# Kernel tuning notes

Measured on AMD Instinct MI355X. Metric: run time of the kernel, lower is better.

The kernel has to match this reference:

```python
import jax, jax.numpy as jnp
import numpy as np

N = 100000
E = 1600000
D_IN = 128
D_HID = 128
D_OUT = 128


def _glorot(key, shape):
    fan_in, fan_out = shape[1], shape[0]
    lim = np.sqrt(6.0 / (fan_in + fan_out)).astype(np.float32)
    return jax.random.uniform(key, shape, jnp.float32, -lim, lim)


def setup_inputs() -> dict:
    key = jax.random.key(0)
    ks = jax.random.split(key, 8)
    x = jax.random.normal(ks[0], (N, D_IN), jnp.float32)
    edge_index = jax.random.randint(ks[1], (2, E), 0, N, jnp.int64)
    # SAGEConv params: lin_l acts on aggregated neighbors (has bias), lin_r on root.
    W1l = _glorot(ks[2], (D_HID, D_IN))
    W1r = _glorot(ks[3], (D_HID, D_IN))
    b1 = jnp.zeros((D_HID,), jnp.float32)
    W2l = _glorot(ks[4], (D_OUT, D_HID))
    W2r = _glorot(ks[5], (D_OUT, D_HID))
    b2 = jnp.zeros((D_OUT,), jnp.float32)
    return {"x": x, "edge_index": edge_index,
            "W1l": W1l, "W1r": W1r, "b1": b1,
            "W2l": W2l, "W2r": W2r, "b2": b2}


def _sage_conv(x, src, dst, Wl, Wr, b):
    # mean-aggregate neighbor features j->i, then lin_l(mean) + lin_r(x) + b
    msgs = x[src]                                             # [E, d]
    summed = jax.ops.segment_sum(msgs, dst, num_segments=N)   # [N, d]
    deg = jax.ops.segment_sum(jnp.ones((src.shape[0],), x.dtype), dst,
                              num_segments=N)                 # [N]
    mean = summed / jnp.maximum(deg, 1.0)[:, None]
    return mean @ Wl.T + x @ Wr.T + b


def reference(x, edge_index, W1l, W1r, b1, W2l, W2r, b2):
    src, dst = edge_index[0], edge_index[1]
    h = jax.nn.relu(_sage_conv(x, src, dst, W1l, W1r, b1))
    # dropout p=0.2 is identity in eval mode
    out = _sage_conv(h, src, dst, W2l, W2r, b2)
    return out
```

## Files before the change

### kernel.cpp

```cpp
#include <hip/hip_runtime.h>
#include <hip/hip_bf16.h>

#define N_NODES 100000
#define N_EDGES 1600000
#define D 128
#define NBUCK 782
#define BSTRIDE 2560
#define EPB 4096

typedef __attribute__((ext_vector_type(8))) short short8v;
typedef __attribute__((ext_vector_type(4))) float f32x4;

__device__ __forceinline__ unsigned short f2bf(float f) {
    unsigned int u = __float_as_uint(f);
    unsigned int r = (u + 0x7fffu + ((u >> 16) & 1u)) >> 16;
    return (unsigned short)r;
}
__device__ __forceinline__ float bf2f(unsigned int lo16) {
    return __uint_as_float(lo16 << 16);
}
__device__ __forceinline__ short8v zero8() {
    short8v z = {0, 0, 0, 0, 0, 0, 0, 0};
    return z;
}
__device__ __forceinline__ short8v cvt8(const float4 p0, const float4 p1) {
    union { __hip_bfloat162 h[4]; short8v s; } u;
    u.h[0] = __float22bfloat162_rn(make_float2(p0.x, p0.y));
    u.h[1] = __float22bfloat162_rn(make_float2(p0.z, p0.w));
    u.h[2] = __float22bfloat162_rn(make_float2(p1.x, p1.y));
    u.h[3] = __float22bfloat162_rn(make_float2(p1.z, p1.w));
    return u.s;
}

__global__ __launch_bounds__(256) void k_bscatter(const int* __restrict__ src,
                                                  const int* __restrict__ dst,
                                                  int* __restrict__ gcnt,
                                                  unsigned int* __restrict__ ebuf) {
    __shared__ int cnt[NBUCK];
    __shared__ int base[NBUCK];
    const int t = threadIdx.x;
    const int e0 = blockIdx.x * EPB;
    for (int i = t; i < NBUCK; i += 256) cnt[i] = 0;
    __syncthreads();
    unsigned int pay[16];
    int meta[16];
#pragma unroll
    for (int u = 0; u < 16; ++u) {
        int e = e0 + u * 256 + t;
        if (e < N_EDGES) {
            int d = dst[e];
            int b = d >> 7;
            int r = atomicAdd(&cnt[b], 1);
            meta[u] = (b << 16) | r;
            pay[u] = ((unsigned int)(d & 127) << 17) | (unsigned int)src[e];
        } else meta[u] = -1;
    }
    __syncthreads();
    for (int i = t; i < NBUCK; i += 256) {
        int c = cnt[i];
        base[i] = c ? atomicAdd(&gcnt[i], c) : 0;
    }
    __syncthreads();
#pragma unroll
    for (int u = 0; u < 16; ++u) {
        if (meta[u] >= 0) {
            int b = meta[u] >> 16;
            int r = meta[u] & 0xffff;
            ebuf[b * BSTRIDE + base[b] + r] = pay[u];
        }
    }
}

__global__ __launch_bounds__(256) void k_bsort(const unsigned int* __restrict__ ebuf,
                                               const int* __restrict__ gcnt,
                                               int* __restrict__ row_start,
                                               int* __restrict__ ssrc) {
    __shared__ int h[128];
    __shared__ int sc[128];
    const int b = blockIdx.x;
    const int t = threadIdx.x;
    const int eb = b * BSTRIDE;
    const int n = gcnt[b];
    if (t < 128) h[t] = 0;
    __syncthreads();
    unsigned int pay[BSTRIDE / 256];
    int meta[BSTRIDE / 256];
#pragma unroll
    for (int u = 0; u < BSTRIDE / 256; ++u) {
        int e = t + u * 256;
        if (e < n) {
            unsigned int pk = ebuf[eb + e];
            int dl = pk >> 17;
            int r = atomicAdd(&h[dl], 1);
            meta[u] = (dl << 16) | r;
            pay[u] = pk;
        } else meta[u] = -1;
    }
    __syncthreads();
    if (t < 128) sc[t] = h[t];
    __syncthreads();
    for (int o = 1; o < 128; o <<= 1) {
        int add = 0;
        if (t < 128 && t >= o) add = sc[t - o];
        __syncthreads();
        if (t < 128) sc[t] += add;
        __syncthreads();
    }
    if (t < 128) {
        int excl = sc[t] - h[t];
        row_start[b * 129 + t] = eb + excl;
        sc[t] = excl;
    }
    if (t == 0) row_start[b * 129 + 128] = eb + n;
    __syncthreads();
#pragma unroll
    for (int u = 0; u < BSTRIDE / 256; ++u) {
        if (meta[u] >= 0) {
            int dl = meta[u] >> 16;
            int r = meta[u] & 0xffff;
            ssrc[eb + sc[dl] + r] = (int)(pay[u] & 0x1ffffu);
        }
    }
}

__global__ __launch_bounds__(256) void k_gemm1(
    const float* __restrict__ Af,
    const float* __restrict__ W1l, const float* __restrict__ W1r,
    const float* __restrict__ bias,
    unsigned short* __restrict__ Tout,
    unsigned short* __restrict__ Hout)
{
    const int wid = threadIdx.x >> 6;
    const int lane = threadIdx.x & 63;
    const int l15 = lane & 15, lg = lane >> 4;
    const int col_base = wid * 64;

    short8v bfrag[4][4];
#pragma unroll
    for (int cg = 0; cg < 4; ++cg) {
        const int row = col_base + cg * 16 + l15;
        const float* wrow = (row < 128) ? &W1l[(size_t)row * 128]
                                        : &W1r[(size_t)(row - 128) * 128];
#pragma unroll
        for (int ks = 0; ks < 4; ++ks) {
            const int k0 = ks * 32 + lg * 8;
            bfrag[cg][ks] = cvt8(*(const float4*)&wrow[k0],
                                 *(const float4*)&wrow[k0 + 4]);
        }
    }
    float bv[4];
#pragma unroll
    for (int cg = 0; cg < 4; ++cg)
        bv[cg] = (wid >= 2) ? bias[(wid - 2) * 64 + cg * 16 + l15] : 0.0f;

    const int row0 = blockIdx.x * 64;
    f32x4 acc[4][4];
#pragma unroll
    for (int rg = 0; rg < 4; ++rg)
#pragma unroll
        for (int cg = 0; cg < 4; ++cg)
            acc[rg][cg] = (f32x4){0.f, 0.f, 0.f, 0.f};

#pragma unroll
    for (int rg = 0; rg < 4; ++rg) {
        const int arow = row0 + rg * 16 + l15;
        short8v afrag[4];
        if (arow < N_NODES) {
#pragma unroll
            for (int ks = 0; ks < 4; ++ks)
                afrag[ks] = cvt8(*(const float4*)&Af[(size_t)arow * 128 + ks * 32 + lg * 8],
                                 *(const float4*)&Af[(size_t)arow * 128 + ks * 32 + lg * 8 + 4]);
        } else {
#pragma unroll
            for (int ks = 0; ks < 4; ++ks) afrag[ks] = zero8();
        }
#pragma unroll
        for (int cg = 0; cg < 4; ++cg)
#pragma unroll
            for (int ks = 0; ks < 4; ++ks)
                acc[rg][cg] = __builtin_amdgcn_mfma_f32_16x16x32_bf16(
                    afrag[ks], bfrag[cg][ks], acc[rg][cg], 0, 0, 0);
    }

    unsigned short* outp = (wid < 2) ? Tout : Hout;
    const int cb = (wid < 2) ? col_base : col_base - 128;
    const bool addb = (wid >= 2);
#pragma unroll
    for (int rg = 0; rg < 4; ++rg) {
        const int rbase = row0 + rg * 16 + lg * 4;
#pragma unroll
        for (int cg = 0; cg < 4; ++cg) {
            const int col = cb + cg * 16 + l15;
#pragma unroll
            for (int i = 0; i < 4; ++i) {
                int row = rbase + i;
                if (row < N_NODES) {
                    float v = acc[rg][cg][i] + (addb ? bv[cg] : 0.0f);
                    *(__hip_bfloat16*)&outp[(size_t)row * 128 + col] = __float2bfloat16(v);
                }
            }
        }
    }
}

__global__ __launch_bounds__(256) void k_gemm2(
    const unsigned short* __restrict__ M,
    const unsigned short* __restrict__ H,
    const float* __restrict__ W2l, const float* __restrict__ W2r,
    const float* __restrict__ bias,
    float* __restrict__ out)
{
    const int wid = threadIdx.x >> 6;
    const int lane = threadIdx.x & 63;
    const int l15 = lane & 15, lg = lane >> 4;
    const int col_base = wid * 32;

    short8v bfrag[2][8];
#pragma unroll
    for (int cg = 0; cg < 2; ++cg) {
        const int o = col_base + cg * 16 + l15;
        const float* wl = &W2l[(size_t)o * 128];
        const float* wr = &W2r[(size_t)o * 128];
#pragma unroll
        for (int ks = 0; ks < 4; ++ks) {
            const int k0 = ks * 32 + lg * 8;
            bfrag[cg][ks]     = cvt8(*(const float4*)&wl[k0], *(const float4*)&wl[k0 + 4]);
            bfrag[cg][ks + 4] = cvt8(*(const float4*)&wr[k0], *(const float4*)&wr[k0 + 4]);
        }
    }
    float bv[2];
#pragma unroll
    for (int cg = 0; cg < 2; ++cg)
        bv[cg] = bias[col_base + cg * 16 + l15];

    const int row0 = blockIdx.x * 64;
    f32x4 acc[4][2];
#pragma unroll
    for (int rg = 0; rg < 4; ++rg)
#pragma unroll
        for (int cg = 0; cg < 2; ++cg)
            acc[rg][cg] = (f32x4){0.f, 0.f, 0.f, 0.f};

#pragma unroll
    for (int rg = 0; rg < 4; ++rg) {
        const int arow = row0 + rg * 16 + l15;
        short8v afrag[8];
        if (arow < N_NODES) {
#pragma unroll
            for (int ks = 0; ks < 4; ++ks) {
                afrag[ks]     = *(const short8v*)&M[(size_t)arow * 128 + ks * 32 + lg * 8];
                afrag[ks + 4] = *(const short8v*)&H[(size_t)arow * 128 + ks * 32 + lg * 8];
            }
        } else {
#pragma unroll
            for (int ks = 0; ks < 8; ++ks) afrag[ks] = zero8();
        }
#pragma unroll
        for (int cg = 0; cg < 2; ++cg)
#pragma unroll
            for (int ks = 0; ks < 8; ++ks)
                acc[rg][cg] = __builtin_amdgcn_mfma_f32_16x16x32_bf16(
                    afrag[ks], bfrag[cg][ks], acc[rg][cg], 0, 0, 0);
    }

#pragma unroll
    for (int rg = 0; rg < 4; ++rg) {
        const int rbase = row0 + rg * 16 + lg * 4;
#pragma unroll
        for (int cg = 0; cg < 2; ++cg) {
            const int col = col_base + cg * 16 + l15;
#pragma unroll
            for (int i = 0; i < 4; ++i) {
                int row = rbase + i;
                if (row < N_NODES)
                    out[(size_t)row * 128 + col] = acc[rg][cg][i] + bv[cg];
            }
        }
    }
}

template <bool RMW>
__global__ __launch_bounds__(256) void k_agg(
    const unsigned short* __restrict__ t_mat,
    const int* __restrict__ ssrc,
    const int* __restrict__ row_start,
    unsigned short* __restrict__ io)
{
    int w = (blockIdx.x * blockDim.x + threadIdx.x) >> 6;
    int lane = threadIdx.x & 63;
    if (w >= N_NODES) return;
    const int b = w >> 7, dl = w & 127;
    const int rs = row_start[b * 129 + dl];
    const int re = row_start[b * 129 + dl + 1];
    const int d = re - rs;
    const int half = lane >> 5;
    const int l31 = lane & 31;

    uint2 cur;
    cur.x = 0u; cur.y = 0u;
    if (RMW && lane < 32)
        cur = *((const uint2*)io + (size_t)w * 32 + l31);

    const uint2* tlane = (const uint2*)t_mat + l31;
    float a0 = 0.f, a1 = 0.f, a2 = 0.f, a3 = 0.f;

    for (int q0 = rs; q0 < re; q0 += 64) {
        int nb = 0;
        if (q0 + lane < re) nb = ssrc[q0 + lane];
        const int m = min(64, re - q0);
        int q = 0;
        for (; q + 16 <= m; q += 16) {
            uint2 v[8];
#pragma unroll
            for (int u = 0; u < 8; ++u) {
                int j = __shfl(nb, q + u * 2 + half);
                v[u] = tlane[(size_t)j * 32];
            }
#pragma unroll
            for (int u = 0; u < 8; ++u) {
                a0 += bf2f(v[u].x & 0xffffu);
                a1 += __uint_as_float(v[u].x & 0xffff0000u);
                a2 += bf2f(v[u].y & 0xffffu);
                a3 += __uint_as_float(v[u].y & 0xffff0000u);
            }
        }
        for (; q + 2 <= m; q += 2) {
            int j = __shfl(nb, q + half);
            uint2 vv = tlane[(size_t)j * 32];
            a0 += bf2f(vv.x & 0xffffu);
            a1 += __uint_as_float(vv.x & 0xffff0000u);
            a2 += bf2f(vv.y & 0xffffu);
            a3 += __uint_as_float(vv.y & 0xffff0000u);
        }
        if (q < m) {
            int j = __shfl(nb, q);
            if (half == 0) {
                uint2 vv = tlane[(size_t)j * 32];
                a0 += bf2f(vv.x & 0xffffu);
                a1 += __uint_as_float(vv.x & 0xffff0000u);
                a2 += bf2f(vv.y & 0xffffu);
                a3 += __uint_as_float(vv.y & 0xffff0000u);
            }
        }
    }

    a0 += __shfl_xor(a0, 32);
    a1 += __shfl_xor(a1, 32);
    a2 += __shfl_xor(a2, 32);
    a3 += __shfl_xor(a3, 32);

    if (lane < 32) {
        const float inv = 1.0f / (float)max(d, 1);
        float r0, r1, r2, r3;
        if (RMW) {
            r0 = fmaxf(bf2f(cur.x & 0xffffu) + inv * a0, 0.f);
            r1 = fmaxf(__uint_as_float(cur.x & 0xffff0000u) + inv * a1, 0.f);
            r2 = fmaxf(bf2f(cur.y & 0xffffu) + inv * a2, 0.f);
            r3 = fmaxf(__uint_as_float(cur.y & 0xffff0000u) + inv * a3, 0.f);
        } else {
            r0 = inv * a0; r1 = inv * a1; r2 = inv * a2; r3 = inv * a3;
        }
        uint2 o;
        o.x = (unsigned int)f2bf(r0) | ((unsigned int)f2bf(r1) << 16);
        o.y = (unsigned int)f2bf(r2) | ((unsigned int)f2bf(r3) << 16);
        *((uint2*)io + (size_t)w * 32 + l31) = o;
    }
}


extern "C" void kernel_launch(void* const* d_in, const int* in_sizes, int n_in,
                              void* d_out, int out_size, void* d_ws, size_t ws_size,
                              hipStream_t stream) {
    const float* x   = (const float*)d_in[0];
    const int*   ei  = (const int*)d_in[1];
    const float* W1l = (const float*)d_in[2];
    const float* W1r = (const float*)d_in[3];
    const float* b1  = (const float*)d_in[4];
    const float* W2l = (const float*)d_in[5];
    const float* W2r = (const float*)d_in[6];
    const float* b2  = (const float*)d_in[7];
    float* out = (float*)d_out;

    const int* src = ei;
    const int* dst = ei + N_EDGES;

    char* p = (char*)d_ws;
    auto alloc = [&](size_t bytes) {
        char* r = p;
        p += (bytes + 255) & ~(size_t)255;
        return r;
    };
    unsigned short* tb = (unsigned short*)alloc((size_t)N_NODES * D * 2);
    unsigned short* hx = (unsigned short*)alloc((size_t)N_NODES * D * 2);
    unsigned int*   ebuf = (unsigned int*)alloc((size_t)NBUCK * BSTRIDE * 4);
    int*   ssrc      = (int*)alloc((size_t)NBUCK * BSTRIDE * 4);
    int*   gcnt      = (int*)alloc(NBUCK * sizeof(int));
    int*   row_start = (int*)alloc((size_t)NBUCK * 129 * sizeof(int));

    const int g1_tiles = (N_NODES + 63) / 64;
    const int agg_grid = (N_NODES + 3) / 4;

    hipMemsetAsync(gcnt, 0, NBUCK * sizeof(int), stream);
    k_bscatter<<<(N_EDGES + EPB - 1) / EPB, 256, 0, stream>>>(src, dst, gcnt, ebuf);
    k_bsort<<<NBUCK, 256, 0, stream>>>(ebuf, gcnt, row_start, ssrc);

    k_gemm1<<<g1_tiles, 256, 0, stream>>>(x, W1l, W1r, b1, tb, hx);
    k_agg<true><<<agg_grid, 256, 0, stream>>>(tb, ssrc, row_start, hx);

    k_agg<false><<<agg_grid, 256, 0, stream>>>(hx, ssrc, row_start, tb);
    k_gemm2<<<g1_tiles, 256, 0, stream>>>(tb, hx, W2l, W2r, b2, out);
}
```

Before: 283.6 us.

## Pre-convert weights to bf16 once and make GEMM kernels persistent

Adds a prep kernel that converts the W1/W2 weights to packed bf16 buffers once and also zeroes the bucket counters, replacing the memset. The two GEMM kernels now load ready bf16 fragments instead of converting fp32 weights in every block. Both kernels become grid-stride persistent loops over 640 blocks, so each block loads its weight fragments once and reuses them across many row tiles. The costs are one extra kernel launch and less parallelism per GEMM launch.

After: 247.6 us, median of 2. 1.15x faster.

```diff
diff --git a/kernel.cpp b/kernel.cpp
--- a/kernel.cpp
+++ b/kernel.cpp
@@ -30,6 +30,22 @@
     u.h[2] = __float22bfloat162_rn(make_float2(p1.x, p1.y));
     u.h[3] = __float22bfloat162_rn(make_float2(p1.z, p1.w));
     return u.s;
+}
+
+__global__ void k_prep(const float* __restrict__ W1l, const float* __restrict__ W1r,
+                       const float* __restrict__ W2l, const float* __restrict__ W2r,
+                       unsigned short* __restrict__ wc1, unsigned short* __restrict__ wc2,
+                       int* __restrict__ gcnt) {
+    int idx = blockIdx.x * 256 + threadIdx.x;
+    if (idx < 16384)       wc1[idx] = f2bf(W1l[idx]);
+    else if (idx < 32768)  wc1[idx] = f2bf(W1r[idx - 16384]);
+    else if (idx < 65536) {
+        int j = idx - 32768;
+        int o = j >> 8, k2 = j & 255;
+        float v = (k2 < 128) ? W2l[o * 128 + k2] : W2r[o * 128 + (k2 - 128)];
+        wc2[j] = f2bf(v);
+    }
+    else if (idx - 65536 < NBUCK) gcnt[idx - 65536] = 0;
 }
 
 __global__ __launch_bounds__(256) void k_bscatter(const int* __restrict__ src,
@@ -125,7 +141,7 @@
 
 __global__ __launch_bounds__(256) void k_gemm1(
     const float* __restrict__ Af,
-    const float* __restrict__ W1l, const float* __restrict__ W1r,
+    const unsigned short* __restrict__ Bt,
     const float* __restrict__ bias,
     unsigned short* __restrict__ Tout,
     unsigned short* __restrict__ Hout)
@@ -137,66 +153,63 @@
 
     short8v bfrag[4][4];
 #pragma unroll
-    for (int cg = 0; cg < 4; ++cg) {
-        const int row = col_base + cg * 16 + l15;
-        const float* wrow = (row < 128) ? &W1l[(size_t)row * 128]
-                                        : &W1r[(size_t)(row - 128) * 128];
-#pragma unroll
-        for (int ks = 0; ks < 4; ++ks) {
-            const int k0 = ks * 32 + lg * 8;
-            bfrag[cg][ks] = cvt8(*(const float4*)&wrow[k0],
-                                 *(const float4*)&wrow[k0 + 4]);
-        }
-    }
+    for (int cg = 0; cg < 4; ++cg)
+#pragma unroll
+        for (int ks = 0; ks < 4; ++ks)
+            bfrag[cg][ks] = *(const short8v*)&Bt[(size_t)(col_base + cg * 16 + l15) * 128
+                                                 + ks * 32 + lg * 8];
     float bv[4];
 #pragma unroll
     for (int cg = 0; cg < 4; ++cg)
         bv[cg] = (wid >= 2) ? bias[(wid - 2) * 64 + cg * 16 + l15] : 0.0f;
 
-    const int row0 = blockIdx.x * 64;
-    f32x4 acc[4][4];
-#pragma unroll
-    for (int rg = 0; rg < 4; ++rg)
-#pragma unroll
-        for (int cg = 0; cg < 4; ++cg)
-            acc[rg][cg] = (f32x4){0.f, 0.f, 0.f, 0.f};
-
-#pragma unroll
-    for (int rg = 0; rg < 4; ++rg) {
-        const int arow = row0 + rg * 16 + l15;
-        short8v afrag[4];
-        if (arow < N_NODES) {
-#pragma unroll
-            for (int ks = 0; ks < 4; ++ks)
-                afrag[ks] = cvt8(*(const float4*)&Af[(size_t)arow * 128 + ks * 32 + lg * 8],
-                                 *(const float4*)&Af[(size_t)arow * 128 + ks * 32 + lg * 8 + 4]);
-        } else {
-#pragma unroll
-            for (int ks = 0; ks < 4; ++ks) afrag[ks] = zero8();
-        }
-#pragma unroll
-        for (int cg = 0; cg < 4; ++cg)
-#pragma unroll
-            for (int ks = 0; ks < 4; ++ks)
-                acc[rg][cg] = __builtin_amdgcn_mfma_f32_16x16x32_bf16(
-                    afrag[ks], bfrag[cg][ks], acc[rg][cg], 0, 0, 0);
-    }
-
-    unsigned short* outp = (wid < 2) ? Tout : Hout;
-    const int cb = (wid < 2) ? col_base : col_base - 128;
-    const bool addb = (wid >= 2);
-#pragma unroll
-    for (int rg = 0; rg < 4; ++rg) {
-        const int rbase = row0 + rg * 16 + lg * 4;
-#pragma unroll
-        for (int cg = 0; cg < 4; ++cg) {
-            const int col = cb + cg * 16 + l15;
-#pragma unroll
-            for (int i = 0; i < 4; ++i) {
-                int row = rbase + i;
-                if (row < N_NODES) {
-                    float v = acc[rg][cg][i] + (addb ? bv[cg] : 0.0f);
-                    *(__hip_bfloat16*)&outp[(size_t)row * 128 + col] = __float2bfloat16(v);
+    const int ntiles = (N_NODES + 63) / 64;
+    for (int tile = blockIdx.x; tile < ntiles; tile += gridDim.x) {
+        const int row0 = tile * 64;
+        f32x4 acc[4][4];
+#pragma unroll
+        for (int rg = 0; rg < 4; ++rg)
+#pragma unroll
+            for (int cg = 0; cg < 4; ++cg)
+                acc[rg][cg] = (f32x4){0.f, 0.f, 0.f, 0.f};
+
+#pragma unroll
+        for (int rg = 0; rg < 4; ++rg) {
+            const int arow = row0 + rg * 16 + l15;
+            short8v afrag[4];
+            if (arow < N_NODES) {
+#pragma unroll
+                for (int ks = 0; ks < 4; ++ks)
+                    afrag[ks] = cvt8(*(const float4*)&Af[(size_t)arow * 128 + ks * 32 + lg * 8],
+                                     *(const float4*)&Af[(size_t)arow * 128 + ks * 32 + lg * 8 + 4]);
+            } else {
+#pragma unroll
+                for (int ks = 0; ks < 4; ++ks) afrag[ks] = zero8();
+            }
+#pragma unroll
+            for (int cg = 0; cg < 4; ++cg)
+#pragma unroll
+                for (int ks = 0; ks < 4; ++ks)
+                    acc[rg][cg] = __builtin_amdgcn_mfma_f32_16x16x32_bf16(
+                        afrag[ks], bfrag[cg][ks], acc[rg][cg], 0, 0, 0);
+        }
+
+        unsigned short* outp = (wid < 2) ? Tout : Hout;
+        const int cb = (wid < 2) ? col_base : col_base - 128;
+        const bool addb = (wid >= 2);
+#pragma unroll
+        for (int rg = 0; rg < 4; ++rg) {
+            const int rbase = row0 + rg * 16 + lg * 4;
+#pragma unroll
+            for (int cg = 0; cg < 4; ++cg) {
+                const int col = cb + cg * 16 + l15;
+#pragma unroll
+                for (int i = 0; i < 4; ++i) {
+                    int row = rbase + i;
+                    if (row < N_NODES) {
+                        float v = acc[rg][cg][i] + (addb ? bv[cg] : 0.0f);
+                        outp[(size_t)row * 128 + col] = f2bf(v);
+                    }
                 }
             }
         }
@@ -206,7 +219,7 @@
 __global__ __launch_bounds__(256) void k_gemm2(
     const unsigned short* __restrict__ M,
     const unsigned short* __restrict__ H,
-    const float* __restrict__ W2l, const float* __restrict__ W2r,
+    const unsigned short* __restrict__ Bt,
     const float* __restrict__ bias,
     float* __restrict__ out)
 {
@@ -217,63 +230,60 @@
 
     short8v bfrag[2][8];
 #pragma unroll
-    for (int cg = 0; cg < 2; ++cg) {
-        const int o = col_base + cg * 16 + l15;
-        const float* wl = &W2l[(size_t)o * 128];
-        const float* wr = &W2r[(size_t)o * 128];
-#pragma unroll
-        for (int ks = 0; ks < 4; ++ks) {
-            const int k0 = ks * 32 + lg * 8;
-            bfrag[cg][ks]     = cvt8(*(const float4*)&wl[k0], *(const float4*)&wl[k0 + 4]);
-            bfrag[cg][ks + 4] = cvt8(*(const float4*)&wr[k0], *(const float4*)&wr[k0 + 4]);
-        }
-    }
+    for (int cg = 0; cg < 2; ++cg)
+#pragma unroll
+        for (int ks = 0; ks < 8; ++ks)
+            bfrag[cg][ks] = *(const short8v*)&Bt[(size_t)(col_base + cg * 16 + l15) * 256
+                                                 + ks * 32 + lg * 8];
     float bv[2];
 #pragma unroll
     for (int cg = 0; cg < 2; ++cg)
         bv[cg] = bias[col_base + cg * 16 + l15];
 
-    const int row0 = blockIdx.x * 64;
-    f32x4 acc[4][2];
-#pragma unroll
-    for (int rg = 0; rg < 4; ++rg)
-#pragma unroll
-        for (int cg = 0; cg < 2; ++cg)
-            acc[rg][cg] = (f32x4){0.f, 0.f, 0.f, 0.f};
-
-#pragma unroll
-    for (int rg = 0; rg < 4; ++rg) {
-        const int arow = row0 + rg * 16 + l15;
-        short8v afrag[8];
-        if (arow < N_NODES) {
-#pragma unroll
-            for (int ks = 0; ks < 4; ++ks) {
-                afrag[ks]     = *(const short8v*)&M[(size_t)arow * 128 + ks * 32 + lg * 8];
-                afrag[ks + 4] = *(const short8v*)&H[(size_t)arow * 128 + ks * 32 + lg * 8];
-            }
-        } else {
-#pragma unroll
-            for (int ks = 0; ks < 8; ++ks) afrag[ks] = zero8();
-        }
-#pragma unroll
-        for (int cg = 0; cg < 2; ++cg)
-#pragma unroll
-            for (int ks = 0; ks < 8; ++ks)
-                acc[rg][cg] = __builtin_amdgcn_mfma_f32_16x16x32_bf16(
-                    afrag[ks], bfrag[cg][ks], acc[rg][cg], 0, 0, 0);
-    }
-
-#pragma unroll
-    for (int rg = 0; rg < 4; ++rg) {
-        const int rbase = row0 + rg * 16 + lg * 4;
-#pragma unroll
-        for (int cg = 0; cg < 2; ++cg) {
-            const int col = col_base + cg * 16 + l15;
-#pragma unroll
-            for (int i = 0; i < 4; ++i) {
-                int row = rbase + i;
-                if (row < N_NODES)
-                    out[(size_t)row * 128 + col] = acc[rg][cg][i] + bv[cg];
+    const int ntiles = (N_NODES + 63) / 64;
+    for (int tile = blockIdx.x; tile < ntiles; tile += gridDim.x) {
+        const int row0 = tile * 64;
+        f32x4 acc[4][2];
+#pragma unroll
+        for (int rg = 0; rg < 4; ++rg)
+#pragma unroll
+            for (int cg = 0; cg < 2; ++cg)
+                acc[rg][cg] = (f32x4){0.f, 0.f, 0.f, 0.f};
+
+#pragma unroll
+        for (int rg = 0; rg < 4; ++rg) {
+            const int arow = row0 + rg * 16 + l15;
+            short8v afrag[8];
+            if (arow < N_NODES) {
+#pragma unroll
+                for (int ks = 0; ks < 4; ++ks) {
+                    afrag[ks]     = *(const short8v*)&M[(size_t)arow * 128 + ks * 32 + lg * 8];
+                    afrag[ks + 4] = *(const short8v*)&H[(size_t)arow * 128 + ks * 32 + lg * 8];
+                }
+            } else {
+#pragma unroll
+                for (int ks = 0; ks < 8; ++ks) afrag[ks] = zero8();
+            }
+#pragma unroll
+            for (int cg = 0; cg < 2; ++cg)
+#pragma unroll
+                for (int ks = 0; ks < 8; ++ks)
+                    acc[rg][cg] = __builtin_amdgcn_mfma_f32_16x16x32_bf16(
+                        afrag[ks], bfrag[cg][ks], acc[rg][cg], 0, 0, 0);
+        }
+
+#pragma unroll
+        for (int rg = 0; rg < 4; ++rg) {
+            const int rbase = row0 + rg * 16 + lg * 4;
+#pragma unroll
+            for (int cg = 0; cg < 2; ++cg) {
+                const int col = col_base + cg * 16 + l15;
+#pragma unroll
+                for (int i = 0; i < 4; ++i) {
+                    int row = rbase + i;
+                    if (row < N_NODES)
+                        out[(size_t)row * 128 + col] = acc[rg][cg][i] + bv[cg];
+                }
             }
         }
     }
@@ -396,17 +406,18 @@
     int*   ssrc      = (int*)alloc((size_t)NBUCK * BSTRIDE * 4);
     int*   gcnt      = (int*)alloc(NBUCK * sizeof(int));
     int*   row_start = (int*)alloc((size_t)NBUCK * 129 * sizeof(int));
-
-    const int g1_tiles = (N_NODES + 63) / 64;
+    unsigned short* wc1 = (unsigned short*)alloc(256 * 128 * 2);
+    unsigned short* wc2 = (unsigned short*)alloc(128 * 256 * 2);
+
     const int agg_grid = (N_NODES + 3) / 4;
 
-    hipMemsetAsync(gcnt, 0, NBUCK * sizeof(int), stream);
+    k_prep<<<(65536 + NBUCK + 255) / 256, 256, 0, stream>>>(W1l, W1r, W2l, W2r, wc1, wc2, gcnt);
     k_bscatter<<<(N_EDGES + EPB - 1) / EPB, 256, 0, stream>>>(src, dst, gcnt, ebuf);
     k_bsort<<<NBUCK, 256, 0, stream>>>(ebuf, gcnt, row_start, ssrc);
 
-    k_gemm1<<<g1_tiles, 256, 0, stream>>>(x, W1l, W1r, b1, tb, hx);
+    k_gemm1<<<640, 256, 0, stream>>>(x, wc1, b1, tb, hx);
     k_agg<true><<<agg_grid, 256, 0, stream>>>(tb, ssrc, row_start, hx);
 
     k_agg<false><<<agg_grid, 256, 0, stream>>>(hx, ssrc, row_start, tb);
-    k_gemm2<<<g1_tiles, 256, 0, stream>>>(tb, hx, W2l, W2r, b2, out);
-}
+    k_gemm2<<<640, 256, 0, stream>>>(tb, hx, wc2, b2, out);
+}
```
